# Performance work log

Hardware: AMD Instinct MI355X
Metric: run time of the kernel (lower is better)

Reference implementation:

```python
import jax, jax.numpy as jnp
import numpy as np

B_SZ, T, D_MODEL, N_STATE = 4, 4096, 1024, 256
D_FF = ((int(8 / 3 * D_MODEL) + 7) // 8) * 8  # 2736
EPS = 1e-6


def setup_inputs() -> dict:
    key = jax.random.key(0)
    ks = jax.random.split(key, 8)
    return {
        "x": jax.random.normal(ks[0], (B_SZ, T, D_MODEL), dtype=jnp.float32),
        "log_lambda": jax.random.normal(ks[1], (N_STATE,), dtype=jnp.float32) * 0.5 + 3.0,
        "B_w": jax.random.normal(ks[2], (N_STATE, D_MODEL), dtype=jnp.float32) / np.sqrt(D_MODEL),
        "C_w": jax.random.normal(ks[3], (D_MODEL, N_STATE), dtype=jnp.float32) / np.sqrt(N_STATE),
        "D_skip": jnp.zeros((D_MODEL,), dtype=jnp.float32),
        "ssm_norm_w": jnp.ones((D_MODEL,), dtype=jnp.float32),
        "ffn_norm_w": jnp.ones((D_MODEL,), dtype=jnp.float32),
        "w1": jax.random.normal(ks[4], (D_FF, D_MODEL), dtype=jnp.float32) / np.sqrt(D_MODEL),
        "w2": jax.random.normal(ks[5], (D_MODEL, D_FF), dtype=jnp.float32) / np.sqrt(D_FF),
        "w3": jax.random.normal(ks[6], (D_FF, D_MODEL), dtype=jnp.float32) / np.sqrt(D_MODEL),
    }


def _rmsnorm(x, w):
    rms = jnp.sqrt(jnp.mean(x * x, axis=-1, keepdims=True) + EPS)
    return x / rms * w


def reference(x, log_lambda, B_w, C_w, D_skip, ssm_norm_w, ffn_norm_w, w1, w2, w3):
    # --- SSM branch ---
    u = _rmsnorm(x, ssm_norm_w)                       # [B,T,D]
    lam = jax.nn.sigmoid(log_lambda)                  # [N]
    Bu = jnp.einsum("btd,nd->btn", u, B_w)            # [B,T,N]

    def step(h, bu_t):                                 # h: [B,N], bu_t: [B,N]
        h = lam * h + bu_t
        return h, h

    h0 = jnp.zeros((x.shape[0], log_lambda.shape[0]), dtype=x.dtype)
    _, hs = jax.lax.scan(step, h0, jnp.swapaxes(Bu, 0, 1))  # hs: [T,B,N]
    hs = jnp.swapaxes(hs, 0, 1)                        # [B,T,N]
    y = jnp.einsum("btn,dn->btd", hs, C_w) + D_skip * u
    x = x + y

    # --- FFN branch (SwiGLU) ---
    z = _rmsnorm(x, ffn_norm_w)
    gate = jax.nn.silu(jnp.einsum("btd,fd->btf", z, w1))
    val = jnp.einsum("btd,fd->btf", z, w3)
    ffn = jnp.einsum("btf,df->btd", gate * val, w2)
    return x + ffn
```

## Files before the change

kernel.cpp:

```cpp
#include <hip/hip_runtime.h>
#include <hip/hip_bf16.h>
#include <cstdint>

#define BSZ   4
#define TLEN  4096
#define DM    1024
#define NS    256
#define DFF   2736
#define DFFP  2816
#define NPK   5632
#define NCHUNK 64
#define CLEN   64

typedef __attribute__((ext_vector_type(8))) short bf16x8;
typedef __attribute__((ext_vector_type(4))) float f32x4;

__device__ __forceinline__ float bf2f(ushort u) {
  union { unsigned int i; float f; } v; v.i = ((unsigned int)u) << 16; return v.f;
}
__device__ __forceinline__ ushort f2bf(float f) {
  union { float f; unsigned int i; } v; v.f = f;
  unsigned int r = v.i + 0x7FFFu + ((v.i >> 16) & 1u);
  return (ushort)(r >> 16);
}
__device__ __forceinline__ void gload16(const ushort* g, ushort* l) {
  __builtin_amdgcn_global_load_lds((const __attribute__((address_space(1))) void*)g,
                                   (__attribute__((address_space(3))) void*)l, 16, 0, 0);
}

__global__ void convert_pad(const float* __restrict__ src, ushort* __restrict__ dst,
                            int srcR, int srcC, int dstR, int dstC) {
  long total = (long)dstR * dstC / 4;
  for (long q = (long)blockIdx.x * blockDim.x + threadIdx.x; q < total;
       q += (long)gridDim.x * blockDim.x) {
    long e = q * 4;
    int r = (int)(e / dstC);
    int c = (int)(e % dstC);
    ushort4 o;
    float v0 = (r < srcR && c + 0 < srcC) ? src[(long)r * srcC + c + 0] : 0.f;
    float v1 = (r < srcR && c + 1 < srcC) ? src[(long)r * srcC + c + 1] : 0.f;
    float v2 = (r < srcR && c + 2 < srcC) ? src[(long)r * srcC + c + 2] : 0.f;
    float v3 = (r < srcR && c + 3 < srcC) ? src[(long)r * srcC + c + 3] : 0.f;
    o.x = f2bf(v0); o.y = f2bf(v1); o.z = f2bf(v2); o.w = f2bf(v3);
    *(ushort4*)(dst + e) = o;
  }
}

__global__ void pack_w13(const float* __restrict__ w1, const float* __restrict__ w3,
                         ushort* __restrict__ wp) {
  long total = (long)NPK * DM / 4;
  for (long q = (long)blockIdx.x * blockDim.x + threadIdx.x; q < total;
       q += (long)gridDim.x * blockDim.x) {
    long e = q * 4;
    int r = (int)(e >> 10);
    int c = (int)(e & 1023);
    int f = ((r >> 5) << 4) + (r & 15);
    const float* src = ((r >> 4) & 1) ? w3 : w1;
    ushort4 o;
    if (f < DFF) {
      const float4 v = *(const float4*)(src + (long)f * DM + c);
      o.x = f2bf(v.x); o.y = f2bf(v.y); o.z = f2bf(v.z); o.w = f2bf(v.w);
    } else {
      o.x = o.y = o.z = o.w = 0;
    }
    *(ushort4*)(wp + e) = o;
  }
}

__global__ __launch_bounds__(256) void rmsnorm_bf16(const float* __restrict__ x,
                                                    const float* __restrict__ w,
                                                    ushort* __restrict__ out) {
  long row = blockIdx.x;
  int tid = threadIdx.x;
  const float4* xr = (const float4*)(x + row * DM);
  float4 v = xr[tid];
  float ss = v.x * v.x + v.y * v.y + v.z * v.z + v.w * v.w;
#pragma unroll
  for (int m = 32; m >= 1; m >>= 1) ss += __shfl_xor(ss, m);
  __shared__ float red[4];
  if ((tid & 63) == 0) red[tid >> 6] = ss;
  __syncthreads();
  float tot = red[0] + red[1] + red[2] + red[3];
  float inv = rsqrtf(tot * (1.0f / DM) + 1e-6f);
  float4 wv = ((const float4*)w)[tid];
  ushort4 o;
  o.x = f2bf(v.x * inv * wv.x);
  o.y = f2bf(v.y * inv * wv.y);
  o.z = f2bf(v.z * inv * wv.z);
  o.w = f2bf(v.w * inv * wv.w);
  ((ushort4*)(out + row * DM))[tid] = o;
}

__global__ __launch_bounds__(256) void scan_local(float* __restrict__ Bu,
                                                  float* __restrict__ E,
                                                  const float* __restrict__ loglam) {
  int bc = blockIdx.x;
  int b = bc / NCHUNK, c = bc % NCHUNK;
  int n = threadIdx.x;
  float lam = 1.f / (1.f + __expf(-loglam[n]));
  float h = 0.f;
  long base = ((long)b * TLEN + (long)c * CLEN) * NS + n;
#pragma unroll 4
  for (int t = 0; t < CLEN; ++t) {
    long idx = base + (long)t * NS;
    h = lam * h + Bu[idx];
    Bu[idx] = h;
  }
  E[((long)b * NCHUNK + c) * NS + n] = h;
}

__global__ __launch_bounds__(1024) void scan_carry(const float* __restrict__ E,
                                                   float* __restrict__ C,
                                                   const float* __restrict__ loglam) {
  int tid = threadIdx.x;
  int b = tid >> 8, n = tid & 255;
  float lam = 1.f / (1.f + __expf(-loglam[n]));
  float lamL = lam;
#pragma unroll
  for (int i = 0; i < 6; ++i) lamL *= lamL;
  float carry = 0.f;
  for (int c = 0; c < NCHUNK; ++c) {
    long idx = ((long)b * NCHUNK + c) * NS + n;
    C[idx] = carry;
    carry = lamL * carry + E[idx];
  }
}

__global__ __launch_bounds__(256) void scan_fix(const float* __restrict__ local,
                                                const float* __restrict__ Carry,
                                                const float* __restrict__ loglam,
                                                ushort* __restrict__ hsb) {
  int bc = blockIdx.x;
  int b = bc / NCHUNK, c = bc % NCHUNK;
  int n = threadIdx.x;
  float lam = 1.f / (1.f + __expf(-loglam[n]));
  float p = Carry[((long)b * NCHUNK + c) * NS + n];
  long base = ((long)b * TLEN + (long)c * CLEN) * NS + n;
#pragma unroll 4
  for (int t = 0; t < CLEN; ++t) {
    p *= lam;
    long idx = base + (long)t * NS;
    hsb[idx] = f2bf(local[idx] + p);
  }
}

template <int EPI>
__global__ __launch_bounds__(256, 2) void gemm_bt(
    const ushort* __restrict__ A, const ushort* __restrict__ B0,
    float* __restrict__ outF,
    const float* __restrict__ xin, const float* __restrict__ dskip,
    const ushort* __restrict__ uin, int M, int N, int K) {
  __shared__ ushort sA[128 * 32];
  __shared__ ushort sB[128 * 32];

  int tid = threadIdx.x;
  int lane = tid & 63;
  int wid = tid >> 6;
  int nbx = N >> 7;
  int by = blockIdx.x / nbx;
  int bx = blockIdx.x - by * nbx;
  long brow = (long)by << 7;
  long bcol = (long)bx << 7;

  int srow = tid >> 2;
  int scol = (tid & 3) << 3;
  const ushort* gA = A + (brow + srow) * (long)K + scol;
  const ushort* gB = B0 + (bcol + srow) * (long)K + scol;
  ushort* lA = sA + (wid << 9);
  ushort* lB = sB + (wid << 9);

  int wr = wid >> 1, wc = wid & 1;
  int fr = lane & 15;
  int fk = (lane >> 4) << 3;

  f32x4 acc0[4][4];
#pragma unroll
  for (int i = 0; i < 4; ++i)
#pragma unroll
    for (int j = 0; j < 4; ++j) acc0[i][j] = (f32x4)0.f;

  long rowq = 64 * (long)K;
  for (int kt = 0; kt < K; kt += 32) {
    __syncthreads();
    gload16(gA + kt, lA);
    gload16(gA + kt + rowq, lA + 2048);
    gload16(gB + kt, lB);
    gload16(gB + kt + rowq, lB + 2048);
    __syncthreads();

    bf16x8 a[4], b[4];
#pragma unroll
    for (int i = 0; i < 4; ++i)
      a[i] = *(const bf16x8*)(sA + ((wr * 64 + i * 16 + fr) * 32 + fk));
#pragma unroll
    for (int j = 0; j < 4; ++j)
      b[j] = *(const bf16x8*)(sB + ((wc * 64 + j * 16 + fr) * 32 + fk));
#pragma unroll
    for (int i = 0; i < 4; ++i)
#pragma unroll
      for (int j = 0; j < 4; ++j)
        acc0[i][j] = __builtin_amdgcn_mfma_f32_16x16x32_bf16(a[i], b[j], acc0[i][j], 0, 0, 0);
  }

#pragma unroll
  for (int i = 0; i < 4; ++i) {
    int rowb = wr * 64 + i * 16 + ((lane >> 4) << 2);
#pragma unroll
    for (int j = 0; j < 4; ++j) {
      long gcol = bcol + wc * 64 + j * 16 + fr;
#pragma unroll
      for (int r = 0; r < 4; ++r) {
        long grow = brow + rowb + r;
        long idx = grow * N + gcol;
        float v = acc0[i][j][r];
        if constexpr (EPI == 0) {
          outF[idx] = v;
        } else {
          outF[idx] = v + xin[idx] + dskip[gcol] * bf2f(uin[idx]);
        }
      }
    }
  }
}

template <bool DUAL>
__global__ __launch_bounds__(512, 2) void big_gemm(
    const ushort* __restrict__ A, const ushort* __restrict__ Bm,
    float* __restrict__ outF, ushort* __restrict__ outU) {
  constexpr int K = DUAL ? DM : DFFP;
  constexpr int N = DUAL ? NPK : DM;
  constexpr int NT = K / 64;
  constexpr int NBX = N / 128;
  constexpr int NWG = 64 * NBX;
  constexpr int BUFE = 24576;
  extern __shared__ __align__(16) char smem_raw[];
  ushort* lds = (ushort*)smem_raw;

  int tid = threadIdx.x;
  int lane = tid & 63;
  int wid = tid >> 6;

  int bid = blockIdx.x;
  int swz = (bid & 7) * (NWG >> 3) + (bid >> 3);
  int by = swz & 63;
  int bx = swz >> 6;
  long brow = (long)by << 8;
  long bcol = (long)bx << 7;

  uint aOff[4]; int aDst[4];
  uint bOff[2]; int bDst[2];
#pragma unroll
  for (int q = 0; q < 4; ++q) {
    int slot = q * 512 + tid;
    int row = slot >> 3, cs = slot & 7;
    int csx = cs ^ (row & 7);
    aOff[q] = (uint)((brow + row) * (long)K + csx * 8);
    aDst[q] = q * 4096 + wid * 512;
  }
#pragma unroll
  for (int q = 0; q < 2; ++q) {
    int slot = q * 512 + tid;
    int row = slot >> 3, cs = slot & 7;
    int csx = cs ^ (row & 7);
    bOff[q] = (uint)((bcol + row) * (long)K + csx * 8);
    bDst[q] = 16384 + q * 4096 + wid * 512;
  }

  int wrm = wid >> 1, wcn = wid & 1;
  int fr = lane & 15, fq = lane >> 4;
  int aAdr[2][4], bAdr[2][4];
#pragma unroll
  for (int kk = 0; kk < 2; ++kk)
#pragma unroll
    for (int i = 0; i < 4; ++i) {
      int row = wrm * 64 + i * 16 + fr;
      aAdr[kk][i] = row * 64 + (((kk * 4 + fq) ^ (row & 7)) << 3);
      int rowb = wcn * 64 + i * 16 + fr;
      bAdr[kk][i] = 16384 + rowb * 64 + (((kk * 4 + fq) ^ (rowb & 7)) << 3);
    }

  auto STAGE = [&](int g, int buf) {
    const ushort* Ag = A + (long)g * 64;
    const ushort* Bg = Bm + (long)g * 64;
    ushort* lb = lds + buf * BUFE;
#pragma unroll
    for (int q = 0; q < 4; ++q) gload16(Ag + aOff[q], lb + aDst[q]);
#pragma unroll
    for (int q = 0; q < 2; ++q) gload16(Bg + bOff[q], lb + bDst[q]);
  };

  f32x4 acc[4][4];
#pragma unroll
  for (int i = 0; i < 4; ++i)
#pragma unroll
    for (int j = 0; j < 4; ++j) acc[i][j] = (f32x4)0.f;

  STAGE(0, 0);
  STAGE(1, 1);
  asm volatile("s_waitcnt vmcnt(6)" ::: "memory");
  asm volatile("s_barrier" ::: "memory");

  int cb = 0, sb = 2;
#pragma unroll 1
  for (int g = 0; g < NT - 2; ++g) {
    const ushort* lb = lds + cb * BUFE;
    bf16x8 a[2][4], b[2][4];
#pragma unroll
    for (int kk = 0; kk < 2; ++kk)
#pragma unroll
      for (int i = 0; i < 4; ++i) {
        a[kk][i] = *(const bf16x8*)(lb + aAdr[kk][i]);
        b[kk][i] = *(const bf16x8*)(lb + bAdr[kk][i]);
      }
    STAGE(g + 2, sb);
#pragma unroll
    for (int kk = 0; kk < 2; ++kk)
#pragma unroll
      for (int i = 0; i < 4; ++i)
#pragma unroll
        for (int j = 0; j < 4; ++j)
          acc[i][j] = __builtin_amdgcn_mfma_f32_16x16x32_bf16(a[kk][i], b[kk][j], acc[i][j], 0, 0, 0);
    asm volatile("s_waitcnt vmcnt(6)" ::: "memory");
    asm volatile("s_barrier" ::: "memory");
    cb = (cb == 2) ? 0 : cb + 1;
    sb = (sb == 2) ? 0 : sb + 1;
  }
  {
    const ushort* lb = lds + cb * BUFE;
    bf16x8 a[2][4], b[2][4];
#pragma unroll
    for (int kk = 0; kk < 2; ++kk)
#pragma unroll
      for (int i = 0; i < 4; ++i) {
        a[kk][i] = *(const bf16x8*)(lb + aAdr[kk][i]);
        b[kk][i] = *(const bf16x8*)(lb + bAdr[kk][i]);
      }
#pragma unroll
    for (int kk = 0; kk < 2; ++kk)
#pragma unroll
      for (int i = 0; i < 4; ++i)
#pragma unroll
        for (int j = 0; j < 4; ++j)
          acc[i][j] = __builtin_amdgcn_mfma_f32_16x16x32_bf16(a[kk][i], b[kk][j], acc[i][j], 0, 0, 0);
    asm volatile("s_waitcnt vmcnt(0)" ::: "memory");
    asm volatile("s_barrier" ::: "memory");
    cb = (cb == 2) ? 0 : cb + 1;
  }
  {
    const ushort* lb = lds + cb * BUFE;
    bf16x8 a[2][4], b[2][4];
#pragma unroll
    for (int kk = 0; kk < 2; ++kk)
#pragma unroll
      for (int i = 0; i < 4; ++i) {
        a[kk][i] = *(const bf16x8*)(lb + aAdr[kk][i]);
        b[kk][i] = *(const bf16x8*)(lb + bAdr[kk][i]);
      }
#pragma unroll
    for (int kk = 0; kk < 2; ++kk)
#pragma unroll
      for (int i = 0; i < 4; ++i)
#pragma unroll
        for (int j = 0; j < 4; ++j)
          acc[i][j] = __builtin_amdgcn_mfma_f32_16x16x32_bf16(a[kk][i], b[kk][j], acc[i][j], 0, 0, 0);
  }

#pragma unroll
  for (int i = 0; i < 4; ++i) {
    int rowb = wrm * 64 + i * 16 + fq * 4;
    if constexpr (DUAL) {
#pragma unroll
      for (int jp = 0; jp < 2; ++jp) {
        int j = jp * 2;
        long fcol = (bcol >> 1) + wcn * 32 + jp * 16 + fr;
#pragma unroll
        for (int r = 0; r < 4; ++r) {
          long grow = brow + rowb + r;
          float gt = acc[i][j][r];
          float vl = acc[i][j + 1][r];
          float s = gt / (1.f + __expf(-gt));
          outU[grow * DFFP + fcol] = f2bf(s * vl);
        }
      }
    } else {
#pragma unroll
      for (int j = 0; j < 4; ++j) {
        long gcol = bcol + wcn * 64 + j * 16 + fr;
#pragma unroll
        for (int r = 0; r < 4; ++r) {
          long grow = brow + rowb + r;
          outF[grow * DM + gcol] += acc[i][j][r];
        }
      }
    }
  }
}

extern "C" void kernel_launch(void* const* d_in, const int* in_sizes, int n_in,
                              void* d_out, int out_size, void* d_ws, size_t ws_size,
                              hipStream_t stream) {
  const float* x      = (const float*)d_in[0];
  const float* loglam = (const float*)d_in[1];
  const float* B_w    = (const float*)d_in[2];
  const float* C_w    = (const float*)d_in[3];
  const float* D_skip = (const float*)d_in[4];
  const float* ssm_w  = (const float*)d_in[5];
  const float* ffn_w  = (const float*)d_in[6];
  const float* w1     = (const float*)d_in[7];
  const float* w2     = (const float*)d_in[8];
  const float* w3     = (const float*)d_in[9];
  float* out = (float*)d_out;

  char* ws = (char*)d_ws;
  ushort* u_bf  = (ushort*)(ws + 0);
  float*  Bu    = (float*) (ws + 33554432);
  ushort* hs_bf = (ushort*)(ws + 50331648);
  float*  E     = (float*) (ws + 58720256);
  float*  Carry = (float*) (ws + 58982400);
  ushort* wB    = (ushort*)(ws + 59244544);
  ushort* wC    = (ushort*)(ws + 59768832);
  ushort* Wp    = (ushort*)(ws + 60293120);
  ushort* w2p   = (ushort*)(ws + 71827456);
  ushort* gv    = (ushort*)(ws + 77594624);

  constexpr int BIG_LDS = 147456;
  (void)hipFuncSetAttribute((const void*)&big_gemm<true>,
                            hipFuncAttributeMaxDynamicSharedMemorySize, BIG_LDS);
  (void)hipFuncSetAttribute((const void*)&big_gemm<false>,
                            hipFuncAttributeMaxDynamicSharedMemorySize, BIG_LDS);

  auto cvb = [](long elems) {
    long q = elems / 4;
    long b = (q + 255) / 256;
    return (int)(b > 4096 ? 4096 : b);
  };

  convert_pad<<<cvb(256L * 1024), 256, 0, stream>>>(B_w, wB, 256, 1024, 256, 1024);
  convert_pad<<<cvb(1024L * 256), 256, 0, stream>>>(C_w, wC, 1024, 256, 1024, 256);
  pack_w13<<<2048, 256, 0, stream>>>(w1, w3, Wp);
  convert_pad<<<cvb(1024L * DFFP), 256, 0, stream>>>(w2, w2p, 1024, DFF, 1024, DFFP);

  rmsnorm_bf16<<<BSZ * TLEN, 256, 0, stream>>>(x, ssm_w, u_bf);
  gemm_bt<0><<<(16384 / 128) * (NS / 128), 256, 0, stream>>>(
      u_bf, wB, Bu, nullptr, nullptr, nullptr, 16384, NS, DM);
  scan_local<<<BSZ * NCHUNK, 256, 0, stream>>>(Bu, E, loglam);
  scan_carry<<<1, 1024, 0, stream>>>(E, Carry, loglam);
  scan_fix<<<BSZ * NCHUNK, 256, 0, stream>>>(Bu, Carry, loglam, hs_bf);
  gemm_bt<1><<<(16384 / 128) * (DM / 128), 256, 0, stream>>>(
      hs_bf, wC, out, x, D_skip, u_bf, 16384, DM, NS);

  rmsnorm_bf16<<<BSZ * TLEN, 256, 0, stream>>>(out, ffn_w, u_bf);
  big_gemm<true><<<64 * (NPK / 128), 512, BIG_LDS, stream>>>(u_bf, Wp, nullptr, gv);
  big_gemm<false><<<64 * (DM / 128), 512, BIG_LDS, stream>>>(gv, w2p, out, nullptr);
}
```

Baseline: 622.6 us.

## Enlarge big GEMM tiles to 256x256 with double-buffered LDS and new block swizzle

The FFN GEMMs move from 256x128 tiles with triple-buffered LDS to 256x256 tiles with double buffering. Each wave now computes a 128x64 sub-tile with 8x4 MFMA accumulators, and block-to-tile mapping is regrouped into 8-row chunks to improve L2 reuse. Larger tiles raise arithmetic intensity and cut redundant global loads. In exchange, register pressure rises (128 accumulator floats per lane, which may break the 2-blocks-per-CU occupancy), the prefetch depth drops to one stage, and there are fewer workgroups (4 per row tile for the w2 GEMM), which hurts wave balance across CUs.

```diff
diff --git a/kernel.cpp b/kernel.cpp
--- a/kernel.cpp
+++ b/kernel.cpp
@@ -228,11 +228,8 @@
     const ushort* __restrict__ A, const ushort* __restrict__ Bm,
     float* __restrict__ outF, ushort* __restrict__ outU) {
   constexpr int K = DUAL ? DM : DFFP;
-  constexpr int N = DUAL ? NPK : DM;
   constexpr int NT = K / 64;
-  constexpr int NBX = N / 128;
-  constexpr int NWG = 64 * NBX;
-  constexpr int BUFE = 24576;
+  constexpr int BUFE = 32768;
   extern __shared__ __align__(16) char smem_raw[];
   ushort* lds = (ushort*)smem_raw;
 
@@ -241,155 +238,110 @@
   int wid = tid >> 6;
 
   int bid = blockIdx.x;
-  int swz = (bid & 7) * (NWG >> 3) + (bid >> 3);
-  int by = swz & 63;
-  int bx = swz >> 6;
-  long brow = (long)by << 8;
-  long bcol = (long)bx << 7;
-
-  uint aOff[4]; int aDst[4];
-  uint bOff[2]; int bDst[2];
+  int chunk = bid & 7;
+  int w = bid >> 3;
+  int rt = chunk * 8 + (w & 7);
+  int ct = w >> 3;
+  long brow = (long)rt << 8;
+  long bcol = (long)ct << 8;
+
+  uint aOff[4], bOff[4];
+  int dstBase[4];
 #pragma unroll
   for (int q = 0; q < 4; ++q) {
     int slot = q * 512 + tid;
     int row = slot >> 3, cs = slot & 7;
     int csx = cs ^ (row & 7);
     aOff[q] = (uint)((brow + row) * (long)K + csx * 8);
-    aDst[q] = q * 4096 + wid * 512;
-  }
-#pragma unroll
-  for (int q = 0; q < 2; ++q) {
-    int slot = q * 512 + tid;
-    int row = slot >> 3, cs = slot & 7;
-    int csx = cs ^ (row & 7);
     bOff[q] = (uint)((bcol + row) * (long)K + csx * 8);
-    bDst[q] = 16384 + q * 4096 + wid * 512;
-  }
-
-  int wrm = wid >> 1, wcn = wid & 1;
+    dstBase[q] = q * 4096 + wid * 512;
+  }
+
+  int wm = wid >> 2, wn = wid & 3;
   int fr = lane & 15, fq = lane >> 4;
-  int aAdr[2][4], bAdr[2][4];
-#pragma unroll
-  for (int kk = 0; kk < 2; ++kk)
-#pragma unroll
-    for (int i = 0; i < 4; ++i) {
-      int row = wrm * 64 + i * 16 + fr;
-      aAdr[kk][i] = row * 64 + (((kk * 4 + fq) ^ (row & 7)) << 3);
-      int rowb = wcn * 64 + i * 16 + fr;
-      bAdr[kk][i] = 16384 + rowb * 64 + (((kk * 4 + fq) ^ (rowb & 7)) << 3);
-    }
+  int abase = (wm * 128 + fr) * 64;
+  int bbase = 16384 + (wn * 64 + fr) * 64;
+  int sl0 = ((0 * 4 + fq) ^ (fr & 7)) << 3;
+  int sl1 = ((1 * 4 + fq) ^ (fr & 7)) << 3;
+
+  f32x4 acc[8][4];
+#pragma unroll
+  for (int m = 0; m < 8; ++m)
+#pragma unroll
+    for (int n = 0; n < 4; ++n) acc[m][n] = (f32x4)0.f;
 
   auto STAGE = [&](int g, int buf) {
     const ushort* Ag = A + (long)g * 64;
     const ushort* Bg = Bm + (long)g * 64;
     ushort* lb = lds + buf * BUFE;
 #pragma unroll
-    for (int q = 0; q < 4; ++q) gload16(Ag + aOff[q], lb + aDst[q]);
-#pragma unroll
-    for (int q = 0; q < 2; ++q) gload16(Bg + bOff[q], lb + bDst[q]);
+    for (int q = 0; q < 4; ++q) gload16(Ag + aOff[q], lb + dstBase[q]);
+#pragma unroll
+    for (int q = 0; q < 4; ++q) gload16(Bg + bOff[q], lb + 16384 + dstBase[q]);
   };
 
-  f32x4 acc[4][4];
-#pragma unroll
-  for (int i = 0; i < 4; ++i)
-#pragma unroll
-    for (int j = 0; j < 4; ++j) acc[i][j] = (f32x4)0.f;
-
   STAGE(0, 0);
-  STAGE(1, 1);
-  asm volatile("s_waitcnt vmcnt(6)" ::: "memory");
-  asm volatile("s_barrier" ::: "memory");
-
-  int cb = 0, sb = 2;
 #pragma unroll 1
-  for (int g = 0; g < NT - 2; ++g) {
-    const ushort* lb = lds + cb * BUFE;
-    bf16x8 a[2][4], b[2][4];
-#pragma unroll
-    for (int kk = 0; kk < 2; ++kk)
-#pragma unroll
-      for (int i = 0; i < 4; ++i) {
-        a[kk][i] = *(const bf16x8*)(lb + aAdr[kk][i]);
-        b[kk][i] = *(const bf16x8*)(lb + bAdr[kk][i]);
-      }
-    STAGE(g + 2, sb);
-#pragma unroll
-    for (int kk = 0; kk < 2; ++kk)
-#pragma unroll
-      for (int i = 0; i < 4; ++i)
-#pragma unroll
-        for (int j = 0; j < 4; ++j)
-          acc[i][j] = __builtin_amdgcn_mfma_f32_16x16x32_bf16(a[kk][i], b[kk][j], acc[i][j], 0, 0, 0);
-    asm volatile("s_waitcnt vmcnt(6)" ::: "memory");
+  for (int g = 0; g < NT; ++g) {
+    if (g + 1 < NT) {
+      STAGE(g + 1, (g + 1) & 1);
+      asm volatile("s_waitcnt vmcnt(8)" ::: "memory");
+    } else {
+      asm volatile("s_waitcnt vmcnt(0)" ::: "memory");
+    }
     asm volatile("s_barrier" ::: "memory");
-    cb = (cb == 2) ? 0 : cb + 1;
-    sb = (sb == 2) ? 0 : sb + 1;
-  }
-  {
-    const ushort* lb = lds + cb * BUFE;
-    bf16x8 a[2][4], b[2][4];
-#pragma unroll
-    for (int kk = 0; kk < 2; ++kk)
-#pragma unroll
-      for (int i = 0; i < 4; ++i) {
-        a[kk][i] = *(const bf16x8*)(lb + aAdr[kk][i]);
-        b[kk][i] = *(const bf16x8*)(lb + bAdr[kk][i]);
-      }
-#pragma unroll
-    for (int kk = 0; kk < 2; ++kk)
-#pragma unroll
-      for (int i = 0; i < 4; ++i)
-#pragma unroll
-        for (int j = 0; j < 4; ++j)
-          acc[i][j] = __builtin_amdgcn_mfma_f32_16x16x32_bf16(a[kk][i], b[kk][j], acc[i][j], 0, 0, 0);
-    asm volatile("s_waitcnt vmcnt(0)" ::: "memory");
+    const ushort* lb = lds + (g & 1) * BUFE;
+    {
+      bf16x8 a[8], b[4];
+#pragma unroll
+      for (int m = 0; m < 8; ++m) a[m] = *(const bf16x8*)(lb + abase + m * 1024 + sl0);
+#pragma unroll
+      for (int n = 0; n < 4; ++n) b[n] = *(const bf16x8*)(lb + bbase + n * 1024 + sl0);
+#pragma unroll
+      for (int m = 0; m < 8; ++m)
+#pragma unroll
+        for (int n = 0; n < 4; ++n)
+          acc[m][n] = __builtin_amdgcn_mfma_f32_16x16x32_bf16(a[m], b[n], acc[m][n], 0, 0, 0);
+    }
+    {
+      bf16x8 a[8], b[4];
+#pragma unroll
+      for (int m = 0; m < 8; ++m) a[m] = *(const bf16x8*)(lb + abase + m * 1024 + sl1);
+#pragma unroll
+      for (int n = 0; n < 4; ++n) b[n] = *(const bf16x8*)(lb + bbase + n * 1024 + sl1);
+#pragma unroll
+      for (int m = 0; m < 8; ++m)
+#pragma unroll
+        for (int n = 0; n < 4; ++n)
+          acc[m][n] = __builtin_amdgcn_mfma_f32_16x16x32_bf16(a[m], b[n], acc[m][n], 0, 0, 0);
+    }
     asm volatile("s_barrier" ::: "memory");
-    cb = (cb == 2) ? 0 : cb + 1;
-  }
-  {
-    const ushort* lb = lds + cb * BUFE;
-    bf16x8 a[2][4], b[2][4];
-#pragma unroll
-    for (int kk = 0; kk < 2; ++kk)
-#pragma unroll
-      for (int i = 0; i < 4; ++i) {
-        a[kk][i] = *(const bf16x8*)(lb + aAdr[kk][i]);
-        b[kk][i] = *(const bf16x8*)(lb + bAdr[kk][i]);
-      }
-#pragma unroll
-    for (int kk = 0; kk < 2; ++kk)
-#pragma unroll
-      for (int i = 0; i < 4; ++i)
-#pragma unroll
-        for (int j = 0; j < 4; ++j)
-          acc[i][j] = __builtin_amdgcn_mfma_f32_16x16x32_bf16(a[kk][i], b[kk][j], acc[i][j], 0, 0, 0);
-  }
-
-#pragma unroll
-  for (int i = 0; i < 4; ++i) {
-    int rowb = wrm * 64 + i * 16 + fq * 4;
+  }
+
+#pragma unroll
+  for (int m = 0; m < 8; ++m) {
+    int rowb = wm * 128 + m * 16 + fq * 4;
     if constexpr (DUAL) {
 #pragma unroll
       for (int jp = 0; jp < 2; ++jp) {
-        int j = jp * 2;
-        long fcol = (bcol >> 1) + wcn * 32 + jp * 16 + fr;
+        long fcol = (bcol >> 1) + wn * 32 + jp * 16 + fr;
 #pragma unroll
         for (int r = 0; r < 4; ++r) {
           long grow = brow + rowb + r;
-          float gt = acc[i][j][r];
-          float vl = acc[i][j + 1][r];
+          float gt = acc[m][2 * jp][r];
+          float vl = acc[m][2 * jp + 1][r];
           float s = gt / (1.f + __expf(-gt));
           outU[grow * DFFP + fcol] = f2bf(s * vl);
         }
       }
     } else {
 #pragma unroll
-      for (int j = 0; j < 4; ++j) {
-        long gcol = bcol + wcn * 64 + j * 16 + fr;
+      for (int n = 0; n < 4; ++n) {
+        long gcol = bcol + wn * 64 + n * 16 + fr;
 #pragma unroll
         for (int r = 0; r < 4; ++r) {
           long grow = brow + rowb + r;
-          outF[grow * DM + gcol] += acc[i][j][r];
+          outF[grow * DM + gcol] += acc[m][n][r];
         }
       }
     }
@@ -423,7 +375,7 @@
   ushort* w2p   = (ushort*)(ws + 71827456);
   ushort* gv    = (ushort*)(ws + 77594624);
 
-  constexpr int BIG_LDS = 147456;
+  constexpr int BIG_LDS = 131072;
   (void)hipFuncSetAttribute((const void*)&big_gemm<true>,
                             hipFuncAttributeMaxDynamicSharedMemorySize, BIG_LDS);
   (void)hipFuncSetAttribute((const void*)&big_gemm<false>,
@@ -450,6 +402,6 @@
       hs_bf, wC, out, x, D_skip, u_bf, 16384, DM, NS);
 
   rmsnorm_bf16<<<BSZ * TLEN, 256, 0, stream>>>(out, ffn_w, u_bf);
-  big_gemm<true><<<64 * (NPK / 128), 512, BIG_LDS, stream>>>(u_bf, Wp, nullptr, gv);
-  big_gemm<false><<<64 * (DM / 128), 512, BIG_LDS, stream>>>(gv, w2p, out, nullptr);
-}
+  big_gemm<true><<<8 * 8 * (NPK / 256), 512, BIG_LDS, stream>>>(u_bf, Wp, nullptr, gv);
+  big_gemm<false><<<8 * 8 * (DM / 256), 512, BIG_LDS, stream>>>(gv, w2p, out, nullptr);
+}
```

Result: faster. 561.4 us (-9.8%).
